# Performance work log

Measured on AMD Instinct MI355X. Metric: run time of the kernel, lower is better.

Reference implementation:

```python
import jax, jax.numpy as jnp
import numpy as np
import math

N = 100000      # active voxels
K = 27          # 3**3 kernel offsets
L = 50000
INC = 64
OUTC = 64


def setup_inputs() -> dict:
    key = jax.random.key(0)
    k1, k2, k3, k4 = jax.random.split(key, 4)
    features = jax.random.normal(k1, (N, INC), dtype=jnp.float32)
    # kernel init: uniform(-std, std), std = 1/sqrt(inc * k^3)
    std = 1.0 / math.sqrt(INC * K)
    kernel = jax.random.uniform(k2, (K, INC, OUTC), dtype=jnp.float32,
                                minval=-std, maxval=std)
    neighbor_in = jax.random.randint(k3, (K, L), 0, N, dtype=jnp.int32)
    neighbor_out = jax.random.randint(k4, (K, L), 0, N, dtype=jnp.int32)
    return {"features": features, "kernel": kernel,
            "neighbor_in": neighbor_in, "neighbor_out": neighbor_out}


def reference(features, kernel, neighbor_in, neighbor_out):
    # gather -> per-offset GEMM -> scatter-add (torchsparse sparseconv_op, transpose=False)
    gathered = features[neighbor_in]                      # [K, L, INC]
    vals = jnp.einsum('klc,kco->klo', gathered, kernel)    # [K, L, OUTC]
    out = jnp.zeros((features.shape[0], kernel.shape[-1]), dtype=features.dtype)
    out = out.at[neighbor_out.reshape(-1)].add(vals.reshape(-1, kernel.shape[-1]))
    return out
```

## Files before the change

kernel.cpp:

```cpp
#include <hip/hip_runtime.h>
#include <hip/hip_bf16.h>


typedef __bf16 bf16x8 __attribute__((ext_vector_type(8)));
typedef float f32x4 __attribute__((ext_vector_type(4)));

#define KOFF 27
#define SLOTK 4
#define NSLOT (KOFF * SLOTK)
#define OVFCAP 8192
#define WPAD 72
#define WTILE (64 * WPAD)
#define KCH 7
#define ROWCHUNK 8192
#define NIBW (ROWCHUNK / 8)

__global__ __launch_bounds__(256) void kA_rank_cast(
    const float* __restrict__ feat, const float* __restrict__ kern,
    const int* __restrict__ nout, __bf16* __restrict__ fb,
    __bf16* __restrict__ wt, unsigned short* __restrict__ slots,
    int2* __restrict__ ovf, int* __restrict__ ovfcnt, int Lpairs, int nElems,
    int nchunk, int rankBlocks, int wtBlocks) {
  __shared__ unsigned int nib[NIBW];
  if ((int)blockIdx.x < rankBlocks) {
    const int k = blockIdx.x / nchunk;
    const int chunk = blockIdx.x % nchunk;
    const int lo = chunk * ROWCHUNK;
    const int tid = threadIdx.x;
    for (int i = tid; i < NIBW; i += 256) nib[i] = 0u;
    __syncthreads();
    const int* nk = nout + k * Lpairs;
    for (int base = 0; base < Lpairs; base += 2048) {
      int l[8], row[8];
#pragma unroll
      for (int j = 0; j < 8; ++j) {
        l[j] = base + j * 256 + tid;
        row[j] = (l[j] < Lpairs) ? nk[l[j]] : -1;
      }
#pragma unroll
      for (int j = 0; j < 8; ++j) {
        int rr = row[j] - lo;
        if (rr >= 0 && rr < ROWCHUNK) {
          unsigned int sh = ((unsigned)rr & 7u) * 4u;
          unsigned int old = atomicAdd(&nib[rr >> 3], 1u << sh);
          int rank = (old >> sh) & 15;
          if (rank < SLOTK) {
            slots[(size_t)row[j] * NSLOT + k * SLOTK + rank] =
                (unsigned short)l[j];
          } else {
            int idx = atomicAdd(ovfcnt, 1);
            if (idx < OVFCAP) ovf[idx] = make_int2(row[j], k * Lpairs + l[j]);
          }
        }
      }
    }
  } else if ((int)blockIdx.x < rankBlocks + wtBlocks) {
    int kc = (blockIdx.x - rankBlocks) * 256 + threadIdx.x;
    if (kc < KOFF * 64) {
      int k = kc >> 6, c = kc & 63;
      const float* src = kern + k * 4096 + c;
      __bf16* dst = wt + (size_t)kc * 64;
#pragma unroll
      for (int i0 = 0; i0 < 64; i0 += 8) {
        bf16x8 v;
#pragma unroll
        for (int q = 0; q < 8; ++q) v[q] = (__bf16)src[(i0 + q) * 64];
        *(bf16x8*)(dst + i0) = v;
      }
    }
  } else {
    int i = ((blockIdx.x - rankBlocks - wtBlocks) * 256 + threadIdx.x) * 8;
    if (i < nElems) {
      f32x4 a = *(const f32x4*)(feat + i);
      f32x4 b = *(const f32x4*)(feat + i + 4);
      bf16x8 v;
#pragma unroll
      for (int j = 0; j < 4; ++j) {
        v[j] = (__bf16)a[j];
        v[j + 4] = (__bf16)b[j];
      }
      *(bf16x8*)(fb + i) = v;
    }
  }
}

__global__ __launch_bounds__(512) void kF_fused(
    const __bf16* __restrict__ fb, const __bf16* __restrict__ wt,
    const int* __restrict__ nin, const unsigned short* __restrict__ slots,
    float* __restrict__ out, int Lpairs, int Nrows) {
  __shared__ __bf16 ldsW[KCH * WTILE];
  const int tid = threadIdx.x;
  const int wv = tid >> 6, lane = tid & 63;
  const int r = lane & 15, g = lane >> 4;
  int row = blockIdx.x * 128 + wv * 16 + r;
  if (row >= Nrows) row = Nrows - 1;
  const unsigned short* srow = slots + (size_t)row * NSLOT;

  const int sc = tid >> 3;
  const int si = (tid & 7) * 8;

  uint2 sv0 = *(const uint2*)(srow);
  uint2 sv1 = *(const uint2*)(srow + SLOTK);
  uint2 sv2 = *(const uint2*)(srow + 2 * SLOTK);
  int e0[4] = {(int)(sv0.x & 0xFFFF), (int)(sv0.x >> 16),
               (int)(sv0.y & 0xFFFF), (int)(sv0.y >> 16)};
  int e1[4] = {(int)(sv1.x & 0xFFFF), (int)(sv1.x >> 16),
               (int)(sv1.y & 0xFFFF), (int)(sv1.y >> 16)};
  int enN[4] = {(int)(sv2.x & 0xFFFF), (int)(sv2.x >> 16),
                (int)(sv2.y & 0xFFFF), (int)(sv2.y >> 16)};
  int irowCur[4], irowNxt[4];
#pragma unroll
  for (int j = 0; j < 4; ++j) irowCur[j] = (e0[j] != 0xFFFF) ? nin[e0[j]] : -1;
  const int* nin1 = nin + Lpairs;
#pragma unroll
  for (int j = 0; j < 4; ++j) irowNxt[j] = (e1[j] != 0xFFFF) ? nin1[e1[j]] : -1;

  f32x4 acc[4] = {f32x4{0.f, 0.f, 0.f, 0.f}, f32x4{0.f, 0.f, 0.f, 0.f},
                  f32x4{0.f, 0.f, 0.f, 0.f}, f32x4{0.f, 0.f, 0.f, 0.f}};

  auto body = [&](int k, int kk) {
    bf16x8 fa[4], fc[4];
#pragma unroll
    for (int j = 0; j < 4; ++j) {
      if (irowCur[j] >= 0) {
        const __bf16* ap = fb + (size_t)irowCur[j] * 64 + g * 8;
        fa[j] = *(const bf16x8*)(ap);
        fc[j] = *(const bf16x8*)(ap + 32);
      }
    }
    const int* nin2 = nin + (size_t)(k + 2) * Lpairs;
    int irowN2[4];
#pragma unroll
    for (int j = 0; j < 4; ++j)
      irowN2[j] = (k + 2 < KOFF && enN[j] != 0xFFFF) ? nin2[enN[j]] : -1;
    uint2 sv3 = make_uint2(0xFFFFFFFFu, 0xFFFFFFFFu);
    if (k + 3 < KOFF) sv3 = *(const uint2*)(srow + (k + 3) * SLOTK);
    float s0[8] = {0.f, 0.f, 0.f, 0.f, 0.f, 0.f, 0.f, 0.f};
    float s1[8] = {0.f, 0.f, 0.f, 0.f, 0.f, 0.f, 0.f, 0.f};
#pragma unroll
    for (int j = 0; j < 4; ++j) {
      if (irowCur[j] >= 0) {
#pragma unroll
        for (int q = 0; q < 8; ++q) {
          s0[q] += (float)fa[j][q];
          s1[q] += (float)fc[j][q];
        }
      }
    }
    bf16x8 b0, b1;
#pragma unroll
    for (int q = 0; q < 8; ++q) {
      b0[q] = (__bf16)s0[q];
      b1[q] = (__bf16)s1[q];
    }
    bf16x8 w0f[4], w1f[4];
#pragma unroll
    for (int t = 0; t < 4; ++t) {
      w0f[t] = *(const bf16x8*)&ldsW[kk * WTILE + (t * 16 + r) * WPAD + g * 8];
      w1f[t] = *(const bf16x8*)&ldsW[kk * WTILE + (t * 16 + r) * WPAD + g * 8 + 32];
    }
#pragma unroll
    for (int t = 0; t < 4; ++t) {
      acc[t] = __builtin_amdgcn_mfma_f32_16x16x32_bf16(w0f[t], b0, acc[t], 0, 0, 0);
      acc[t] = __builtin_amdgcn_mfma_f32_16x16x32_bf16(w1f[t], b1, acc[t], 0, 0, 0);
    }
#pragma unroll
    for (int j = 0; j < 4; ++j) {
      irowCur[j] = irowNxt[j];
      irowNxt[j] = irowN2[j];
    }
    enN[0] = (int)(sv3.x & 0xFFFF);
    enN[1] = (int)(sv3.x >> 16);
    enN[2] = (int)(sv3.y & 0xFFFF);
    enN[3] = (int)(sv3.y >> 16);
  };

  int kbase = 0;
#pragma unroll 1
  for (int c = 0; c < 4; ++c) {
    const int kcnt = (c < 3) ? KCH : (KOFF - 3 * KCH);
    if (c) __syncthreads();
#pragma unroll
    for (int kk = 0; kk < KCH; ++kk) {
      if (kk < kcnt) {
        bf16x8 w = *(const bf16x8*)(wt + (size_t)(kbase + kk) * 4096 + sc * 64 + si);
        *(bf16x8*)&ldsW[kk * WTILE + sc * WPAD + si] = w;
      }
    }
    __syncthreads();
    for (int kk = 0; kk < kcnt; ++kk) body(kbase + kk, kk);
    kbase += kcnt;
  }

  float* op = out + (size_t)row * 64;
#pragma unroll
  for (int t = 0; t < 4; ++t) *(f32x4*)(op + t * 16 + g * 4) = acc[t];
}

__global__ __launch_bounds__(256) void k4_fixup(
    const __bf16* __restrict__ fb, const __bf16* __restrict__ wt,
    const int* __restrict__ nin, const int2* __restrict__ ovf,
    const int* __restrict__ ovfcnt, float* __restrict__ out, int Lpairs) {
  int gid = blockIdx.x * 256 + threadIdx.x;
  int i = gid >> 6, c = gid & 63;
  int n = *ovfcnt;
  if (n > OVFCAP) n = OVFCAP;
  if (i >= n) return;
  int row = ovf[i].x, pid = ovf[i].y;
  int k = pid / Lpairs;
  int irow = nin[pid];
  const __bf16* wk = wt + ((size_t)k * 64 + c) * 64;
  const __bf16* f = fb + (size_t)irow * 64;
  float s = 0.f;
#pragma unroll 8
  for (int q = 0; q < 64; ++q) s += (float)f[q] * (float)wk[q];
  atomicAdd(&out[(size_t)row * 64 + c], s);
}

__global__ __launch_bounds__(256) void spconv_atomic_kernel(
    const float* __restrict__ feat, const float* __restrict__ kern,
    const int* __restrict__ nin, const int* __restrict__ nout,
    float* __restrict__ out, int Lpairs, int blocksPerK) {
  __shared__ __bf16 ldsBT[64 * WPAD];
  const int bk = blockIdx.x / blocksPerK;
  const int chunk = blockIdx.x % blocksPerK;
  const float* kb = kern + bk * 4096;
  for (int idx = threadIdx.x; idx < 4096; idx += 256) {
    int i = idx >> 6, c = idx & 63;
    ldsBT[c * WPAD + i] = (__bf16)kb[idx];
  }
  __syncthreads();
  const int lane = threadIdx.x & 63;
  const int wave = threadIdx.x >> 6;
  const int r = lane & 15, g = lane >> 4;
  bf16x8 bfrag[2][4];
#pragma unroll
  for (int s = 0; s < 2; ++s)
#pragma unroll
    for (int t = 0; t < 4; ++t)
      bfrag[s][t] = *(const bf16x8*)&ldsBT[(t * 16 + r) * WPAD + g * 8 + s * 32];
  const int* ninK = nin + bk * Lpairs;
  const int* noutK = nout + bk * Lpairs;
  const int base0 = chunk * 512 + wave * 128;
  for (int it = 0; it < 8; ++it) {
    const int base = base0 + it * 16;
    if (base >= Lpairs) break;
    const int arow = ninK[base + r];
    const float* ap = feat + (size_t)arow * 64 + g * 8;
    f32x4 f0 = *(const f32x4*)(ap);
    f32x4 f1 = *(const f32x4*)(ap + 4);
    f32x4 f2 = *(const f32x4*)(ap + 32);
    f32x4 f3 = *(const f32x4*)(ap + 36);
    bf16x8 a0, a1;
#pragma unroll
    for (int j = 0; j < 4; ++j) {
      a0[j] = (__bf16)f0[j];
      a0[j + 4] = (__bf16)f1[j];
      a1[j] = (__bf16)f2[j];
      a1[j + 4] = (__bf16)f3[j];
    }
    f32x4 acc[4] = {f32x4{0.f, 0.f, 0.f, 0.f}, f32x4{0.f, 0.f, 0.f, 0.f},
                    f32x4{0.f, 0.f, 0.f, 0.f}, f32x4{0.f, 0.f, 0.f, 0.f}};
#pragma unroll
    for (int t = 0; t < 4; ++t) {
      acc[t] = __builtin_amdgcn_mfma_f32_16x16x32_bf16(a0, bfrag[0][t], acc[t], 0, 0, 0);
      acc[t] = __builtin_amdgcn_mfma_f32_16x16x32_bf16(a1, bfrag[1][t], acc[t], 0, 0, 0);
    }
    int orow[4];
#pragma unroll
    for (int reg = 0; reg < 4; ++reg) orow[reg] = noutK[base + g * 4 + reg];
#pragma unroll
    for (int t = 0; t < 4; ++t)
#pragma unroll
      for (int reg = 0; reg < 4; ++reg)
        atomicAdd(out + (size_t)orow[reg] * 64 + t * 16 + r, acc[t][reg]);
  }
}

extern "C" void kernel_launch(void* const* d_in, const int* in_sizes, int n_in,
                              void* d_out, int out_size, void* d_ws, size_t ws_size,
                              hipStream_t stream) {
  const float* feat = (const float*)d_in[0];
  const float* kern = (const float*)d_in[1];
  const int* nin = (const int*)d_in[2];
  const int* nout = (const int*)d_in[3];
  float* out = (float*)d_out;

  const int total = in_sizes[2];
  const int Lpairs = total / KOFF;
  const int Nrows = out_size / 64;
  const int nElems = Nrows * 64;

  const size_t slotsBytes = (size_t)Nrows * NSLOT * 2;
  const size_t ovfOff = (slotsBytes + 255) & ~(size_t)255;
  const size_t cntOff = (ovfOff + (size_t)OVFCAP * 8 + 255) & ~(size_t)255;
  const size_t wtOff = (cntOff + 256 + 255) & ~(size_t)255;
  const size_t fbOff = (wtOff + (size_t)KOFF * 4096 * 2 + 255) & ~(size_t)255;
  const size_t needed = fbOff + (size_t)nElems * 2;

  const bool shapeOK = (Lpairs <= 65535) && (Lpairs % 16 == 0) &&
                       (total % KOFF == 0) && (out_size % 64 == 0);

  if (shapeOK && ws_size >= needed) {
    unsigned short* slots = (unsigned short*)d_ws;
    int2* ovf = (int2*)((char*)d_ws + ovfOff);
    int* ovfcnt = (int*)((char*)d_ws + cntOff);
    __bf16* wt = (__bf16*)((char*)d_ws + wtOff);
    __bf16* fb = (__bf16*)((char*)d_ws + fbOff);

    hipMemsetAsync(slots, 0xFF, slotsBytes, stream);
    hipMemsetAsync(ovfcnt, 0, 4, stream);

    const int nchunk = (Nrows + ROWCHUNK - 1) / ROWCHUNK;
    const int rankBlocks = KOFF * nchunk;
    const int wtBlocks = (KOFF * 64 + 255) / 256;
    const int castBlocks = (nElems / 8 + 255) / 256;
    kA_rank_cast<<<rankBlocks + wtBlocks + castBlocks, 256, 0, stream>>>(
        feat, kern, nout, fb, wt, slots, ovf, ovfcnt, Lpairs, nElems, nchunk,
        rankBlocks, wtBlocks);
    kF_fused<<<(Nrows + 127) / 128, 512, 0, stream>>>(fb, wt, nin, slots, out,
                                                      Lpairs, Nrows);
    k4_fixup<<<OVFCAP * 64 / 256, 256, 0, stream>>>(fb, wt, nin, ovf, ovfcnt,
                                                    out, Lpairs);
  } else {
    const int blocksPerK = (Lpairs + 511) / 512;
    hipMemsetAsync(d_out, 0, (size_t)out_size * sizeof(float), stream);
    spconv_atomic_kernel<<<KOFF * blocksPerK, 256, 0, stream>>>(
        feat, kern, nin, nout, out, Lpairs, blocksPerK);
  }
}
```

Measured before the change: 138.5 us.

## Double-buffer feature gathers one offset ahead and fully unroll offset loop

```diff
diff --git a/kernel.cpp b/kernel.cpp
--- a/kernel.cpp
+++ b/kernel.cpp
@@ -84,7 +84,7 @@
   }
 }
 
-__global__ __launch_bounds__(512) void kF_fused(
+__global__ __launch_bounds__(512, 4) void kF_fused(
     const __bf16* __restrict__ fb, const __bf16* __restrict__ wt,
     const int* __restrict__ nin, const unsigned short* __restrict__ slots,
     float* __restrict__ out, int Lpairs, int Nrows) {
@@ -108,9 +108,10 @@
                (int)(sv1.y & 0xFFFF), (int)(sv1.y >> 16)};
   int enN[4] = {(int)(sv2.x & 0xFFFF), (int)(sv2.x >> 16),
                 (int)(sv2.y & 0xFFFF), (int)(sv2.y >> 16)};
-  int irowCur[4], irowNxt[4];
-#pragma unroll
-  for (int j = 0; j < 4; ++j) irowCur[j] = (e0[j] != 0xFFFF) ? nin[e0[j]] : -1;
+  int irowNxt[4];
+  int gA[4], gB[4];
+#pragma unroll
+  for (int j = 0; j < 4; ++j) gA[j] = (e0[j] != 0xFFFF) ? nin[e0[j]] : -1;
   const int* nin1 = nin + Lpairs;
 #pragma unroll
   for (int j = 0; j < 4; ++j) irowNxt[j] = (e1[j] != 0xFFFF) ? nin1[e1[j]] : -1;
@@ -118,14 +119,26 @@
   f32x4 acc[4] = {f32x4{0.f, 0.f, 0.f, 0.f}, f32x4{0.f, 0.f, 0.f, 0.f},
                   f32x4{0.f, 0.f, 0.f, 0.f}, f32x4{0.f, 0.f, 0.f, 0.f}};
 
-  auto body = [&](int k, int kk) {
-    bf16x8 fa[4], fc[4];
+  bf16x8 faA[4], fcA[4], faB[4], fcB[4];
+#pragma unroll
+  for (int j = 0; j < 4; ++j) {
+    if (gA[j] >= 0) {
+      const __bf16* ap = fb + (size_t)gA[j] * 64 + g * 8;
+      faA[j] = *(const bf16x8*)(ap);
+      fcA[j] = *(const bf16x8*)(ap + 32);
+    }
+  }
+
+  auto body = [&](int k, int kk, bf16x8(&faC)[4], bf16x8(&fcC)[4], int(&gC)[4],
+                  bf16x8(&faN)[4], bf16x8(&fcN)[4], int(&gN)[4]) {
+#pragma unroll
+    for (int j = 0; j < 4; ++j) gN[j] = (k + 1 < KOFF) ? irowNxt[j] : -1;
 #pragma unroll
     for (int j = 0; j < 4; ++j) {
-      if (irowCur[j] >= 0) {
-        const __bf16* ap = fb + (size_t)irowCur[j] * 64 + g * 8;
-        fa[j] = *(const bf16x8*)(ap);
-        fc[j] = *(const bf16x8*)(ap + 32);
+      if (gN[j] >= 0) {
+        const __bf16* ap = fb + (size_t)gN[j] * 64 + g * 8;
+        faN[j] = *(const bf16x8*)(ap);
+        fcN[j] = *(const bf16x8*)(ap + 32);
       }
     }
     const int* nin2 = nin + (size_t)(k + 2) * Lpairs;
@@ -139,11 +152,11 @@
     float s1[8] = {0.f, 0.f, 0.f, 0.f, 0.f, 0.f, 0.f, 0.f};
 #pragma unroll
     for (int j = 0; j < 4; ++j) {
-      if (irowCur[j] >= 0) {
+      if (gC[j] >= 0) {
 #pragma unroll
         for (int q = 0; q < 8; ++q) {
-          s0[q] += (float)fa[j][q];
-          s1[q] += (float)fc[j][q];
+          s0[q] += (float)faC[j][q];
+          s1[q] += (float)fcC[j][q];
         }
       }
     }
@@ -165,19 +178,16 @@
       acc[t] = __builtin_amdgcn_mfma_f32_16x16x32_bf16(w1f[t], b1, acc[t], 0, 0, 0);
     }
 #pragma unroll
-    for (int j = 0; j < 4; ++j) {
-      irowCur[j] = irowNxt[j];
-      irowNxt[j] = irowN2[j];
-    }
+    for (int j = 0; j < 4; ++j) irowNxt[j] = irowN2[j];
     enN[0] = (int)(sv3.x & 0xFFFF);
     enN[1] = (int)(sv3.x >> 16);
     enN[2] = (int)(sv3.y & 0xFFFF);
     enN[3] = (int)(sv3.y >> 16);
   };
 
-  int kbase = 0;
-#pragma unroll 1
+#pragma unroll
   for (int c = 0; c < 4; ++c) {
+    const int kbase = c * KCH;
     const int kcnt = (c < 3) ? KCH : (KOFF - 3 * KCH);
     if (c) __syncthreads();
 #pragma unroll
@@ -188,8 +198,16 @@
       }
     }
     __syncthreads();
-    for (int kk = 0; kk < kcnt; ++kk) body(kbase + kk, kk);
-    kbase += kcnt;
+#pragma unroll
+    for (int kk = 0; kk < KCH; ++kk) {
+      if (kk < kcnt) {
+        const int k = kbase + kk;
+        if ((k & 1) == 0)
+          body(k, kk, faA, fcA, gA, faB, fcB, gB);
+        else
+          body(k, kk, faB, fcB, gB, faA, fcA, gA);
+      }
+    }
   }
 
   float* op = out + (size_t)row * 64;
```

Result: slower. 166.2 us (+20.0%).
